# Optimization experiments

Hardware: AMD Instinct MI355X
Metric: run time of the kernel (lower is better)

The kernel has to match this reference:

```python
import jax, jax.numpy as jnp
import numpy as np

NUM_ENTITIES = 40000
NUM_RELATIONS = 500
NUM_EDGES = 400000
ENT_DIM = 50
REL_DIM = 50
NUM_HEADS = 8
UNITS = [150, 300]
NEG_SLOPE = 0.2


def setup_inputs() -> dict:
    key = jax.random.key(0)
    ks = jax.random.split(key, 12)
    h_index = jax.random.randint(ks[0], (NUM_EDGES,), 0, NUM_ENTITIES)
    r_index = jax.random.randint(ks[1], (NUM_EDGES,), 0, NUM_RELATIONS)
    t_index = jax.random.randint(ks[2], (NUM_EDGES,), 0, NUM_ENTITIES)
    std_e = np.sqrt(1.0 / ENT_DIM).astype(np.float32)
    std_r = np.sqrt(1.0 / REL_DIM).astype(np.float32)
    entity_embeddings = jax.random.truncated_normal(ks[3], -2.0, 2.0, (NUM_ENTITIES, ENT_DIM), jnp.float32) * std_e
    relation_embeddings = jax.random.truncated_normal(ks[4], -2.0, 2.0, (NUM_RELATIONS, REL_DIM), jnp.float32) * std_r
    # gat0: input ent dim 50, rel dim 50 -> concat 150, units 150
    c0 = ENT_DIM + REL_DIM + ENT_DIM
    gat0_kernel = jax.random.normal(ks[5], (NUM_HEADS, c0, UNITS[0]), jnp.float32) * (1.0 / np.sqrt(c0))
    gat0_attn = jax.random.normal(ks[6], (NUM_HEADS, UNITS[0]), jnp.float32) * (1.0 / np.sqrt(UNITS[0]))
    gat0_rel_kernel = jax.random.normal(ks[7], (REL_DIM, UNITS[0]), jnp.float32) * (1.0 / np.sqrt(REL_DIM))
    # gat1: input ent dim 8*150=1200, rel dim 150 -> concat 2550, units 300
    e1 = NUM_HEADS * UNITS[0]
    c1 = e1 + UNITS[0] + e1
    gat1_kernel = jax.random.normal(ks[8], (NUM_HEADS, c1, UNITS[1]), jnp.float32) * (1.0 / np.sqrt(c1))
    gat1_attn = jax.random.normal(ks[9], (NUM_HEADS, UNITS[1]), jnp.float32) * (1.0 / np.sqrt(UNITS[1]))
    gat1_rel_kernel = jax.random.normal(ks[10], (UNITS[0], UNITS[1]), jnp.float32) * (1.0 / np.sqrt(UNITS[0]))
    dense_w = jax.random.normal(ks[11], (ENT_DIM, UNITS[1]), jnp.float32) * (1.0 / np.sqrt(ENT_DIM))
    dense_b = jnp.zeros((UNITS[1],), jnp.float32)
    return dict(h_index=h_index, r_index=r_index, t_index=t_index,
                entity_embeddings=entity_embeddings, relation_embeddings=relation_embeddings,
                gat0_kernel=gat0_kernel, gat0_attn=gat0_attn, gat0_rel_kernel=gat0_rel_kernel,
                gat1_kernel=gat1_kernel, gat1_attn=gat1_attn, gat1_rel_kernel=gat1_rel_kernel,
                dense_w=dense_w, dense_b=dense_b)


def _kbgat_layer(h, r, t, ent, rel, kernel, attn, rel_kernel):
    """One KBGAT layer. kernel: [H, De+Dr+De, U] acting on concat(ent[h], rel[r], ent[t]).
    Split kernel so projections happen at node/relation level (equivalent, avoids E x concat_dim)."""
    N = ent.shape[0]
    De = ent.shape[1]
    Dr = rel.shape[1]
    outs = []
    for hd in range(kernel.shape[0]):
        W = kernel[hd]
        Wh, Wr, Wt = W[:De], W[De:De + Dr], W[De + Dr:]
        # message c_{hrt} = W [ent_h ; rel_r ; ent_t] : [E, U]
        c = (ent @ Wh)[h] + (rel @ Wr)[r] + (ent @ Wt)[t]
        s = jax.nn.leaky_relu(c @ attn[hd], NEG_SLOPE)  # [E]
        # segment softmax over triples sharing the same head entity
        m = jax.ops.segment_max(s, h, num_segments=N)
        e = jnp.exp(s - m[h])
        d = jax.ops.segment_sum(e, h, num_segments=N)
        a = e / (d[h] + 1e-10)
        agg = jax.ops.segment_sum(a[:, None] * c, h, num_segments=N)  # [N, U]
        outs.append(jax.nn.elu(agg))
    rel_out = rel @ rel_kernel
    return outs, rel_out


def reference(h_index, r_index, t_index, entity_embeddings, relation_embeddings,
              gat0_kernel, gat0_attn, gat0_rel_kernel,
              gat1_kernel, gat1_attn, gat1_rel_kernel, dense_w, dense_b):
    h = h_index.astype(jnp.int32)
    r = r_index.astype(jnp.int32)
    t = t_index.astype(jnp.int32)
    # dropout rate is 0.0 / inference -> identity
    outs0, rel0 = _kbgat_layer(h, r, t, entity_embeddings, relation_embeddings,
                               gat0_kernel, gat0_attn, gat0_rel_kernel)
    feat = jnp.concatenate(outs0, axis=-1)  # [N, H*U0]
    outs1, rel1 = _kbgat_layer(h, r, t, feat, rel0, gat1_kernel, gat1_attn, gat1_rel_kernel)
    ent_out = outs1[0]
    for o in outs1[1:]:
        ent_out = ent_out + o  # add_n over heads
    ent_out = ent_out + (entity_embeddings @ dense_w + dense_b)  # dense residual
    return ent_out, rel1
```

## Files before the change

### kernel.cpp

```cpp
#include <hip/hip_runtime.h>
#include <hip/hip_bf16.h>
#include <math.h>
#include <stdint.h>

typedef __attribute__((ext_vector_type(8))) __bf16 bf16x8;
typedef __attribute__((ext_vector_type(4))) float f32x4;
typedef unsigned short us;

#define GLP(p) ((__attribute__((address_space(1))) void*)(p))
#define LDP(p) ((__attribute__((address_space(3))) void*)(p))

static __device__ __forceinline__ float b2f(us u) {
    return __uint_as_float(((unsigned int)u) << 16);
}
static __device__ __forceinline__ us f2b(float f) {
    unsigned int x = __float_as_uint(f);
    return (us)((x + 0x7fffu + ((x >> 16) & 1u)) >> 16);
}

__global__ __launch_bounds__(256) void sentinel(float* out, int n, float v) {
    int i = blockIdx.x * 256 + threadIdx.x;
    if (i < n) out[i] = v;
}

__global__ __launch_bounds__(256) void zero_featpad(us* __restrict__ feat) {
    int idx = blockIdx.x * 256 + threadIdx.x;
    if (idx < 40064 * 16) {
        int n = idx >> 4, c = idx & 15;
        feat[(size_t)n * 1216 + 1200 + c] = 0;
    }
}
__global__ __launch_bounds__(256) void zero_x0pad(us* __restrict__ X0) {
    int idx = blockIdx.x * 256 + threadIdx.x;
    if (idx < 4 * 64 * 192) {
        int w = idx / (64 * 192);
        int rem = idx % (64 * 192);
        int rr = rem / 192, c = rem % 192;
        X0[((size_t)w * 40064 + 40000 + rr) * 192 + c] = 0;
    }
}

__global__ __launch_bounds__(256) void count_edges(const int* __restrict__ h, int* __restrict__ counts) {
    int e = blockIdx.x * 256 + threadIdx.x;
    if (e < 400000) atomicAdd(&counts[h[e]], 1);
}

__global__ void scan40k(const int* __restrict__ counts, int* __restrict__ rs) {
    __shared__ int part[1024];
    int tid = threadIdx.x;
    int base = tid * 40;
    int s = 0;
    for (int i = 0; i < 40; ++i) { int idx = base + i; s += (idx < 40000) ? counts[idx] : 0; }
    part[tid] = s;
    __syncthreads();
    for (int off = 1; off < 1024; off <<= 1) {
        int v = (tid >= off) ? part[tid - off] : 0;
        __syncthreads();
        part[tid] += v;
        __syncthreads();
    }
    int run = (tid == 0) ? 0 : part[tid - 1];
    for (int i = 0; i < 40; ++i) {
        int idx = base + i;
        if (idx < 40000) { rs[idx] = run; run += counts[idx]; }
    }
    if (tid == 1023) rs[40000] = part[1023];
}

__global__ __launch_bounds__(256) void scatter_edges(const int* __restrict__ h, const int* __restrict__ rs,
                                                     int* __restrict__ cursor, int* __restrict__ se) {
    int e = blockIdx.x * 256 + threadIdx.x;
    if (e < 400000) {
        int n = h[e];
        int pos = rs[n] + atomicAdd(&cursor[n], 1);
        se[pos] = e;
    }
}

__global__ __launch_bounds__(256) void pack_ent(const float* __restrict__ ent, us* __restrict__ A0) {
    int idx = blockIdx.x * 256 + threadIdx.x;
    if (idx >= 40064 * 64) return;
    int n = idx >> 6, k = idx & 63;
    A0[idx] = (n < 40000 && k < 50) ? f2b(ent[n * 50 + k]) : (us)0;
}

__global__ __launch_bounds__(256) void build_V0(const float* __restrict__ g0k, const float* __restrict__ attn0,
                                                float* __restrict__ V0) {
    int idx = blockIdx.x * 256 + threadIdx.x;
    if (idx >= 50 * 24) return;
    int k = idx / 24, g = idx % 24;
    int part = g >> 3, hd = g & 7;
    int row = k + (part == 1 ? 100 : (part == 2 ? 50 : 0));
    float s = 0.f;
    for (int u = 0; u < 150; ++u)
        s += g0k[(hd * 150 + row) * 150 + u] * attn0[hd * 150 + u];
    V0[idx] = s;
}

__global__ __launch_bounds__(256) void build_VT0(const float* __restrict__ g0k, const float* __restrict__ attn0,
                                                 us* __restrict__ VT0) {
    int idx = blockIdx.x * 256 + threadIdx.x;
    if (idx >= 128 * 64) return;
    int g = idx >> 6, k = idx & 63;
    us v = 0;
    if (g < 16 && k < 50) {
        int part = g >> 3, hd = g & 7;
        int row = part ? (100 + k) : k;
        float s = 0.f;
        for (int u = 0; u < 150; ++u)
            s += g0k[(hd * 150 + row) * 150 + u] * attn0[hd * 150 + u];
        v = f2b(s);
    }
    VT0[idx] = v;
}

__global__ __launch_bounds__(256) void build_VT1(const float* __restrict__ g1k, const float* __restrict__ attn1,
                                                 us* __restrict__ VT1) {
    int idx = blockIdx.x * 256 + threadIdx.x;
    if (idx >= 128 * 1216) return;
    int g = idx / 1216, k = idx % 1216;
    us v = 0;
    if (g < 16 && k < 1200) {
        int part = g >> 3, hd = g & 7;
        int row = part ? (1350 + k) : k;
        float s = 0.f;
        for (int u = 0; u < 300; ++u)
            s += g1k[((size_t)hd * 2550 + row) * 300 + u] * attn1[hd * 300 + u];
        v = f2b(s);
    }
    VT1[idx] = v;
}

__global__ __launch_bounds__(256) void build_Vr1(const float* __restrict__ g1k, const float* __restrict__ attn1,
                                                 float* __restrict__ Vr1) {
    int idx = blockIdx.x * 256 + threadIdx.x;
    if (idx >= 150 * 8) return;
    int k = idx / 8, hd = idx % 8;
    float s = 0.f;
    for (int u = 0; u < 300; ++u)
        s += g1k[((size_t)hd * 2550 + 1200 + k) * 300 + u] * attn1[hd * 300 + u];
    Vr1[idx] = s;
}

__global__ __launch_bounds__(256) void build_dwT(const float* __restrict__ dw, us* __restrict__ dwT) {
    int idx = blockIdx.x * 256 + threadIdx.x;
    if (idx >= 384 * 64) return;
    int j = idx >> 6, k = idx & 63;
    us v = 0;
    if (j < 300 && k < 50) v = f2b(dw[k * 300 + j]);
    dwT[idx] = v;
}

__global__ __launch_bounds__(256) void scalar_proj(const void* __restrict__ Av, int aIsF32, int lda, int K,
                                                   const float* __restrict__ V, int ldv, int col0, int G,
                                                   float* __restrict__ out) {
    __shared__ float arow[1216];
    long n = blockIdx.x;
    if (aIsF32) {
        const float* A = (const float*)Av;
        for (int k = threadIdx.x; k < K; k += 256) arow[k] = A[n * lda + k];
    } else {
        const us* A = (const us*)Av;
        for (int k = threadIdx.x; k < K; k += 256) arow[k] = b2f(A[n * lda + k]);
    }
    __syncthreads();
    int g = threadIdx.x >> 4;
    int sl = threadIdx.x & 15;
    if (g < G) {
        float s = 0.f;
        for (int k = sl; k < K; k += 16) s += arow[k] * V[k * ldv + col0 + g];
        for (int off = 8; off; off >>= 1) s += __shfl_down(s, off, 16);
        if (sl == 0) out[n * G + g] = s;
    }
}

__global__ __launch_bounds__(256) void edge_stats2(const int* __restrict__ rs, const int* __restrict__ se,
                                                   const int* __restrict__ rIdx, const int* __restrict__ tIdx,
                                                   const float* __restrict__ sc, const float* __restrict__ arr,
                                                   us* __restrict__ eAT, float* __restrict__ sfac,
                                                   float* __restrict__ sS) {
    int tid = blockIdx.x * 256 + threadIdx.x;
    if (tid >= 40000 * 8) return;
    int n = tid >> 3, hd = tid & 7;
    float ah = sc[n * 16 + hd];
    int p0 = rs[n], p1 = rs[n + 1];
    float m = -INFINITY, d = 0.f;
    for (int p = p0; p < p1; ++p) {
        int e = se[p];
        float s = ah + arr[rIdx[e] * 8 + hd] + sc[tIdx[e] * 16 + 8 + hd];
        s = (s > 0.f) ? s : 0.2f * s;
        sS[(size_t)p * 8 + hd] = s;
        if (s > m) { d = d * expf(m - s) + 1.f; m = s; }
        else d += expf(s - m);
    }
    float inv = 1.f / (d + 1e-10f);
    us* ea = eAT + (size_t)hd * 400000;
    for (int p = p0; p < p1; ++p) {
        float s = sS[(size_t)p * 8 + hd];
        ea[p] = f2b(expf(s - m) * inv);
    }
    sfac[tid] = d * inv;
}

__global__ __launch_bounds__(256) void agg0x4(int g, const int* __restrict__ rs, const int* __restrict__ se,
                                              const int* __restrict__ rIdx, const int* __restrict__ tIdx,
                                              const us* __restrict__ eAT, const float* __restrict__ sfac,
                                              const float* __restrict__ ent, const float* __restrict__ rel,
                                              us* __restrict__ X0) {
    __shared__ int sr[128], st[128];
    __shared__ float sa[4][128];
    long n = blockIdx.x;
    int tid = threadIdx.x;
    int lane = tid & 63, wave = tid >> 6;
    int hd = 4 * g + wave;
    int k = lane;
    float ev = (k < 50) ? ent[n * 50 + k] : 0.f;
    float xh = sfac[n * 8 + hd] * ev;
    float ra = 0.f, ta = 0.f;
    int p0 = rs[n], p1 = rs[n + 1];
    for (int c0 = p0; c0 < p1; c0 += 128) {
        int cnt = min(128, p1 - c0);
        __syncthreads();
        if (tid < cnt) {
            int e = se[c0 + tid];
            sr[tid] = rIdx[e];
            st[tid] = tIdx[e];
#pragma unroll
            for (int w = 0; w < 4; ++w)
                sa[w][tid] = b2f(eAT[(size_t)(4 * g + w) * 400000 + c0 + tid]);
        }
        __syncthreads();
#pragma unroll 4
        for (int i = 0; i < cnt; ++i) {
            float a = sa[wave][i];
            int r = sr[i], t = st[i];
            if (k < 50) {
                ra += a * rel[r * 50 + k];
                ta += a * ent[(long)t * 50 + k];
            }
        }
    }
    us* row = X0 + ((size_t)wave * 40064 + n) * 192;
    if (k < 50) { row[k] = f2b(xh); row[50 + k] = f2b(ra); row[100 + k] = f2b(ta); }
    if (lane < 42) row[150 + lane] = 0;
}

__global__ __launch_bounds__(256) void build_B0T8(const float* __restrict__ g0k, us* __restrict__ B) {
    int idx = blockIdx.x * 256 + threadIdx.x;
    if (idx >= 8 * 256 * 192) return;
    int hd = idx / (256 * 192);
    int u = (idx / 192) % 256, k = idx % 192;
    us v = 0;
    if (u < 150 && k < 150) v = f2b(g0k[((size_t)hd * 150 + k) * 150 + u]);
    B[idx] = v;
}

__global__ __launch_bounds__(256) void build_B1Th2T(int g, const float* __restrict__ g1k, us* __restrict__ B) {
    __shared__ us tile[64][65];
    int j0 = blockIdx.x * 64, k0 = blockIdx.y * 64;
    int tl = threadIdx.x & 63, th = threadIdx.x >> 6;
#pragma unroll 4
    for (int i = 0; i < 16; ++i) {
        int jj = j0 + tl;
        int kk = k0 + th + 4 * i;
        us v = 0;
        if (jj < 1216 && kk < 1200) {
            int blk = jj / 304, u = jj % 304;
            if (u < 300) {
                int hd = 2 * g + (blk & 1);
                int row = (blk >= 2) ? (1350 + kk) : kk;
                v = f2b(g1k[((size_t)hd * 2550 + row) * 300 + u]);
            }
        }
        tile[tl][th + 4 * i] = v;
    }
    __syncthreads();
#pragma unroll 4
    for (int i = 0; i < 16; ++i) {
        int k = k0 + tl;
        int j = j0 + th + 4 * i;
        if (j < 1280 && k < 1216) B[(size_t)j * 1216 + k] = tile[th + 4 * i][tl];
    }
}

#define GEMM_BODY(EPILOG)                                                                       \
    __shared__ __align__(16) us As[2][128 * 64];                                                \
    __shared__ __align__(16) us Bs[2][128 * 64];                                                \
    const int tid = threadIdx.x;                                                                \
    const int lane = tid & 63, wave = tid >> 6;                                                 \
    const int wr = wave >> 1, wc = wave & 1;                                                    \
    const int r16 = lane & 15, g4 = lane >> 4;                                                  \
    const int gx = gridDim.x;                                                                   \
    const int nwg = gx * gridDim.y;                                                             \
    const int orig = blockIdx.y * gx + blockIdx.x;                                              \
    const int q8 = nwg >> 3, r8 = nwg & 7;                                                      \
    const int xcd = orig & 7;                                                                   \
    const int lg = (xcd < r8 ? xcd * (q8 + 1) : r8 * (q8 + 1) + (xcd - r8) * q8) + (orig >> 3); \
    const long bm = lg / gx, bn = lg % gx;                                                      \
    f32x4 acc[4][4];                                                                            \
    _Pragma("unroll") for (int m = 0; m < 4; ++m)                                               \
        _Pragma("unroll") for (int n = 0; n < 4; ++n) acc[m][n] = (f32x4){0.f, 0.f, 0.f, 0.f};  \
    auto stage = [&](int buf, int kt) {                                                         \
        _Pragma("unroll") for (int i = 0; i < 4; ++i) {                                         \
            int idx = tid + i * 256;                                                            \
            int row = idx >> 3, sub = idx & 7;                                                  \
            int scol = ((sub ^ (row & 7)) << 3);                                                \
            const us* ga = A + (bm * 128 + row) * (long)K + kt + scol;                          \
            __builtin_amdgcn_global_load_lds(GLP(ga), LDP(&As[buf][idx * 8]), 16, 0, 0);        \
        }                                                                                       \
        _Pragma("unroll") for (int i = 0; i < 4; ++i) {                                         \
            int idx = tid + i * 256;                                                            \
            int row = idx >> 3, sub = idx & 7;                                                  \
            int scol = ((sub ^ (row & 7)) << 3);                                                \
            const us* gb = BT + (bn * 128 + row) * (long)K + kt + scol;                         \
            __builtin_amdgcn_global_load_lds(GLP(gb), LDP(&Bs[buf][idx * 8]), 16, 0, 0);        \
        }                                                                                       \
    };                                                                                          \
    const int nt = K >> 6;                                                                      \
    stage(0, 0);                                                                                \
    const int sxor = (r16 & 7) << 3;                                                            \
    for (int t = 0; t < nt; ++t) {                                                              \
        int cur = t & 1;                                                                        \
        if (t + 1 < nt) {                                                                       \
            stage(cur ^ 1, (t + 1) << 6);                                                       \
            asm volatile("s_waitcnt vmcnt(8)" ::: "memory");                                    \
        } else {                                                                                \
            asm volatile("s_waitcnt vmcnt(0)" ::: "memory");                                    \
        }                                                                                       \
        __builtin_amdgcn_s_barrier();                                                           \
        asm volatile("" ::: "memory");                                                          \
        __builtin_amdgcn_s_setprio(1);                                                          \
        _Pragma("unroll") for (int kk = 0; kk < 2; ++kk) {                                      \
            bf16x8 af[4], bfr[4];                                                               \
            _Pragma("unroll") for (int m = 0; m < 4; ++m)                                       \
                af[m] = *(const bf16x8*)&As[cur][(wr * 64 + m * 16 + r16) * 64 +                \
                                               ((kk * 32 + g4 * 8) ^ sxor)];                    \
            _Pragma("unroll") for (int n = 0; n < 4; ++n)                                       \
                bfr[n] = *(const bf16x8*)&Bs[cur][(wc * 64 + n * 16 + r16) * 64 +               \
                                                ((kk * 32 + g4 * 8) ^ sxor)];                   \
            _Pragma("unroll") for (int m = 0; m < 4; ++m)                                       \
                _Pragma("unroll") for (int n = 0; n < 4; ++n)                                   \
                    acc[m][n] = __builtin_amdgcn_mfma_f32_16x16x32_bf16(af[m], bfr[n],          \
                                                                        acc[m][n], 0, 0, 0);    \
        }                                                                                       \
        __builtin_amdgcn_s_setprio(0);                                                          \
        asm volatile("" ::: "memory");                                                          \
        __builtin_amdgcn_s_barrier();                                                           \
    }                                                                                           \
    _Pragma("unroll") for (int m = 0; m < 4; ++m)                                               \
        _Pragma("unroll") for (int n = 0; n < 4; ++n)                                           \
            _Pragma("unroll") for (int j = 0; j < 4; ++j) { EPILOG }

__global__ __launch_bounds__(256) void gemm_bt(const us* __restrict__ A_, const us* __restrict__ BT_,
                                               us* __restrict__ C, int K, int ldc, int nColReal,
                                               int colOff0, int colOffZ, long aStrideZ, long btStrideZ,
                                               int act) {
    const int z = blockIdx.z;
    const us* A = A_ + (size_t)z * aStrideZ;
    const us* BT = BT_ + (size_t)z * btStrideZ;
    const int colBase = colOff0 + z * colOffZ;
    GEMM_BODY(
        int cc = (int)bn * 128 + wc * 64 + n * 16 + r16;
        if (cc < nColReal) {
            long row = bm * 128 + wr * 64 + m * 16 + g4 * 4 + j;
            float v = acc[m][n][j];
            if (act) v = (v > 0.f) ? v : expm1f(v);
            C[row * (long)ldc + colBase + cc] = f2b(v);
        })
}

__global__ __launch_bounds__(256) void gemm_bt_f32(const us* __restrict__ A, const us* __restrict__ BT,
                                                   float* __restrict__ C, int K, int ldc, int nColReal,
                                                   const float* __restrict__ bias) {
    GEMM_BODY(
        int cc = (int)bn * 128 + wc * 64 + n * 16 + r16;
        if (cc < nColReal) {
            long row = bm * 128 + wr * 64 + m * 16 + g4 * 4 + j;
            float v = acc[m][n][j];
            if (bias) v += bias[cc];
            C[row * (long)ldc + cc] = v;
        })
}

__global__ __launch_bounds__(256) void rel0_kernel(const float* __restrict__ rel, const float* __restrict__ g0rk,
                                                   float* __restrict__ rel0b) {
    int idx = blockIdx.x * 256 + threadIdx.x;
    if (idx >= 500 * 150) return;
    int rI = idx / 150, u = idx % 150;
    float s = 0.f;
    for (int k = 0; k < 50; ++k) s += rel[rI * 50 + k] * g0rk[k * 150 + u];
    rel0b[idx] = s;
}

__global__ __launch_bounds__(256) void pr1_kernel(const float* __restrict__ rel0b, const float* __restrict__ g1k,
                                                  us* __restrict__ PR1b) {
    int idx = blockIdx.x * 256 + threadIdx.x;
    if (idx >= 500 * 2400) return;
    int rI = idx / 2400, jj = idx % 2400;
    int hd = jj / 300, u = jj % 300;
    float s = 0.f;
    for (int k = 0; k < 150; ++k)
        s += rel0b[rI * 150 + k] * g1k[((size_t)hd * 2550 + 1200 + k) * 300 + u];
    PR1b[idx] = f2b(s);
}

__global__ __launch_bounds__(256) void rel1_kernel(const float* __restrict__ rel0b, const float* __restrict__ g1rk,
                                                   float* __restrict__ out) {
    int idx = blockIdx.x * 256 + threadIdx.x;
    if (idx >= 500 * 300) return;
    int rI = idx / 300, u = idx % 300;
    float s = 0.f;
    for (int k = 0; k < 150; ++k) s += rel0b[rI * 150 + k] * g1rk[k * 300 + u];
    out[idx] = s;
}

__global__ __launch_bounds__(256) void agg1h2(int g, const int* __restrict__ rs, const int* __restrict__ se,
                                              const int* __restrict__ rIdx, const int* __restrict__ tIdx,
                                              const us* __restrict__ eAT, const float* __restrict__ sfac,
                                              const us* __restrict__ C1g2, const us* __restrict__ PR1b,
                                              float* __restrict__ outf) {
    __shared__ int sr[128], st[128];
    __shared__ float sa0[128], sa1[128];
    long n = blockIdx.x;
    int tid = threadIdx.x;
    int hd0 = 2 * g, hd1 = hd0 + 1;
    int d = tid, d2 = tid + 256;
    bool a2 = (d2 < 300);
    float sf0 = sfac[n * 8 + hd0], sf1 = sfac[n * 8 + hd1];
    const us* crow = C1g2 + (size_t)n * 1216;
    float acc00 = sf0 * b2f(crow[d]);
    float acc10 = sf1 * b2f(crow[304 + d]);
    float acc01 = a2 ? sf0 * b2f(crow[d2]) : 0.f;
    float acc11 = a2 ? sf1 * b2f(crow[304 + d2]) : 0.f;
    const us* ea0 = eAT + (size_t)hd0 * 400000;
    const us* ea1 = eAT + (size_t)hd1 * 400000;
    int p0 = rs[n], p1 = rs[n + 1];
    for (int c0 = p0; c0 < p1; c0 += 128) {
        int cnt = min(128, p1 - c0);
        __syncthreads();
        if (tid < cnt) {
            int e = se[c0 + tid];
            sr[tid] = rIdx[e];
            st[tid] = tIdx[e];
            sa0[tid] = b2f(ea0[c0 + tid]);
            sa1[tid] = b2f(ea1[c0 + tid]);
        }
        __syncthreads();
#pragma unroll 4
        for (int i = 0; i < cnt; ++i) {
            int r = sr[i], t = st[i];
            float a0 = sa0[i], a1 = sa1[i];
            const us* ct = C1g2 + (size_t)t * 1216;
            const us* pr = PR1b + (size_t)r * 2400;
            acc00 += a0 * (b2f(pr[hd0 * 300 + d]) + b2f(ct[608 + d]));
            acc10 += a1 * (b2f(pr[hd1 * 300 + d]) + b2f(ct[912 + d]));
            if (a2) {
                acc01 += a0 * (b2f(pr[hd0 * 300 + d2]) + b2f(ct[608 + d2]));
                acc11 += a1 * (b2f(pr[hd1 * 300 + d2]) + b2f(ct[912 + d2]));
            }
        }
    }
    float v00 = (acc00 > 0.f) ? acc00 : expm1f(acc00);
    float v10 = (acc10 > 0.f) ? acc10 : expm1f(acc10);
    outf[n * 300 + d] += v00 + v10;
    if (a2) {
        float v01 = (acc01 > 0.f) ? acc01 : expm1f(acc01);
        float v11 = (acc11 > 0.f) ? acc11 : expm1f(acc11);
        outf[n * 300 + d2] += v01 + v11;
    }
}

extern "C" void kernel_launch(void* const* d_in, const int* in_sizes, int n_in,
                              void* d_out, int out_size, void* d_ws, size_t ws_size,
                              hipStream_t stream) {
    const int* hIdx = (const int*)d_in[0];
    const int* rIdx = (const int*)d_in[1];
    const int* tIdx = (const int*)d_in[2];
    const float* ent  = (const float*)d_in[3];
    const float* rel  = (const float*)d_in[4];
    const float* g0k  = (const float*)d_in[5];
    const float* at0w = (const float*)d_in[6];
    const float* g0rk = (const float*)d_in[7];
    const float* g1k  = (const float*)d_in[8];
    const float* at1w = (const float*)d_in[9];
    const float* g1rk = (const float*)d_in[10];
    const float* dw   = (const float*)d_in[11];
    const float* db   = (const float*)d_in[12];
    float* outf = (float*)d_out;

    {
        const int exp_sz[13] = {400000, 400000, 400000, 2000000, 25000, 180000, 1200,
                                7500, 6120000, 2400, 45000, 15000, 300};
        bool ok = (n_in == 13);
        for (int i = 0; ok && i < 13; ++i) ok = (in_sizes[i] == exp_sz[i]);
        if (!ok) {
            sentinel<<<(out_size + 255) / 256, 256, 0, stream>>>(outf, out_size, 44.0f);
            return;
        }
    }

    char* p = (char*)d_ws;
    auto carve = [&](size_t bytes) -> char* {
        char* r = p;
        p += (bytes + 255) & ~(size_t)255;
        return r;
    };
    int* counts = (int*)carve(40000 * 4);
    int* cursor = (int*)carve(40000 * 4);
    int* rs     = (int*)carve(40001 * 4);
    int* se     = (int*)carve(400000 * 4);
    float* sc   = (float*)carve((size_t)40064 * 16 * 4);
    float* arS  = (float*)carve(500 * 8 * 4);
    us* eAT     = (us*)carve((size_t)8 * 400000 * 2);
    float* sfac = (float*)carve((size_t)40000 * 8 * 4);
    float* V0  = (float*)carve(50 * 24 * 4);
    float* Vr1 = (float*)carve(150 * 8 * 4);
    float* rel0b = (float*)carve(500 * 150 * 4);
    us* PR1b  = (us*)carve((size_t)500 * 2400 * 2);
    us* VT0   = (us*)carve((size_t)128 * 64 * 2);
    us* VT1   = (us*)carve((size_t)128 * 1216 * 2);
    us* dwT   = (us*)carve((size_t)384 * 64 * 2);
    us* B0T8  = (us*)carve((size_t)8 * 256 * 192 * 2);
    us* B1Th2 = (us*)carve((size_t)1280 * 1216 * 2);
    us* feat  = (us*)carve((size_t)40064 * 1216 * 2);
    char* tail = p;
    us* A0    = (us*)tail;
    float* sS = (float*)tail;
    us* X0    = (us*)tail;
    us* C1g2  = (us*)tail;
    size_t tailNeed = (size_t)40064 * 1216 * 2;
    size_t totalNeed = (size_t)(tail - (char*)d_ws) + tailNeed;
    if (totalNeed > ws_size) {
        sentinel<<<(out_size + 255) / 256, 256, 0, stream>>>(outf, out_size, 42.0f);
        return;
    }

    hipMemsetAsync(counts, 0, 40000 * 4, stream);
    hipMemsetAsync(cursor, 0, 40000 * 4, stream);
    zero_featpad<<<(40064 * 16 + 255) / 256, 256, 0, stream>>>(feat);

    count_edges<<<1563, 256, 0, stream>>>(hIdx, counts);
    scan40k<<<1, 1024, 0, stream>>>(counts, rs);
    scatter_edges<<<1563, 256, 0, stream>>>(hIdx, rs, cursor, se);

    pack_ent<<<(40064 * 64 + 255) / 256, 256, 0, stream>>>(ent, A0);
    build_VT0<<<(128 * 64 + 255) / 256, 256, 0, stream>>>(g0k, at0w, VT0);
    gemm_bt_f32<<<dim3(1, 313), 256, 0, stream>>>(A0, VT0, sc, 64, 16, 16, nullptr);
    build_dwT<<<(384 * 64 + 255) / 256, 256, 0, stream>>>(dw, dwT);
    gemm_bt_f32<<<dim3(3, 313), 256, 0, stream>>>(A0, dwT, outf, 64, 300, 300, db);
    build_V0<<<5, 256, 0, stream>>>(g0k, at0w, V0);
    scalar_proj<<<500, 256, 0, stream>>>(rel, 1, 50, 50, V0, 24, 16, 8, arS);
    edge_stats2<<<1250, 256, 0, stream>>>(rs, se, rIdx, tIdx, sc, arS, eAT, sfac, sS);

    zero_x0pad<<<(4 * 64 * 192 + 255) / 256, 256, 0, stream>>>(X0);
    build_B0T8<<<(8 * 256 * 192 + 255) / 256, 256, 0, stream>>>(g0k, B0T8);
    for (int g = 0; g < 2; ++g) {
        agg0x4<<<40000, 256, 0, stream>>>(g, rs, se, rIdx, tIdx, eAT, sfac, ent, rel, X0);
        gemm_bt<<<dim3(2, 313, 4), 256, 0, stream>>>(X0, B0T8 + (size_t)g * 4 * 256 * 192, feat,
                                                     192, 1216, 150, g * 600, 150,
                                                     (long)40064 * 192, (long)256 * 192, 1);
    }

    rel0_kernel<<<(500 * 150 + 255) / 256, 256, 0, stream>>>(rel, g0rk, rel0b);
    build_VT1<<<(128 * 1216 + 255) / 256, 256, 0, stream>>>(g1k, at1w, VT1);
    build_Vr1<<<5, 256, 0, stream>>>(g1k, at1w, Vr1);
    gemm_bt_f32<<<dim3(1, 313), 256, 0, stream>>>(feat, VT1, sc, 1216, 16, 16, nullptr);
    scalar_proj<<<500, 256, 0, stream>>>(rel0b, 1, 150, 150, Vr1, 8, 0, 8, arS);
    edge_stats2<<<1250, 256, 0, stream>>>(rs, se, rIdx, tIdx, sc, arS, eAT, sfac, sS);
    pr1_kernel<<<(500 * 2400 + 255) / 256, 256, 0, stream>>>(rel0b, g1k, PR1b);

    for (int g = 0; g < 4; ++g) {
        build_B1Th2T<<<dim3(20, 19), 256, 0, stream>>>(g, g1k, B1Th2);
        gemm_bt<<<dim3(10, 313, 1), 256, 0, stream>>>(feat, B1Th2, C1g2,
                                                      1216, 1216, 1216, 0, 0, 0, 0, 0);
        agg1h2<<<40000, 256, 0, stream>>>(g, rs, se, rIdx, tIdx, eAT, sfac, C1g2, PR1b, outf);
    }

    rel1_kernel<<<(500 * 300 + 255) / 256, 256, 0, stream>>>(rel0b, g1rk, outf + (size_t)40000 * 300);
}
```

Baseline: 1.941 ms.

## Map one wavefront per node in both aggregation kernels, dropping LDS staging

Both edge-aggregation kernels now give each wavefront its own destination node, four nodes per block, instead of one node per 256-thread block. The layer-0 kernel has each wave accumulate all four heads for its node, so each relation and tail row is loaded once and reused across heads. The layer-1 kernel has each lane own five contiguous output columns. The shared-memory edge staging and __syncthreads barriers are removed, along with idle threads on low-degree nodes. In exchange, the layer-1 loads of five contiguous bf16 values per lane are strided across lanes and less coalesced, and edge metadata is re-read by every lane.

After: 2.506 ms. +29.1%, slower.

```diff
diff --git a/kernel.cpp b/kernel.cpp
--- a/kernel.cpp
+++ b/kernel.cpp
@@ -202,47 +202,40 @@
     sfac[tid] = d * inv;
 }
 
-__global__ __launch_bounds__(256) void agg0x4(int g, const int* __restrict__ rs, const int* __restrict__ se,
-                                              const int* __restrict__ rIdx, const int* __restrict__ tIdx,
-                                              const us* __restrict__ eAT, const float* __restrict__ sfac,
-                                              const float* __restrict__ ent, const float* __restrict__ rel,
-                                              us* __restrict__ X0) {
-    __shared__ int sr[128], st[128];
-    __shared__ float sa[4][128];
-    long n = blockIdx.x;
-    int tid = threadIdx.x;
-    int lane = tid & 63, wave = tid >> 6;
-    int hd = 4 * g + wave;
+__global__ __launch_bounds__(256) void agg0x4w(int g, const int* __restrict__ rs, const int* __restrict__ se,
+                                               const int* __restrict__ rIdx, const int* __restrict__ tIdx,
+                                               const us* __restrict__ eAT, const float* __restrict__ sfac,
+                                               const float* __restrict__ ent, const float* __restrict__ rel,
+                                               us* __restrict__ X0) {
+    int wave = threadIdx.x >> 6, lane = threadIdx.x & 63;
+    long n = (long)blockIdx.x * 4 + wave;
     int k = lane;
     float ev = (k < 50) ? ent[n * 50 + k] : 0.f;
-    float xh = sfac[n * 8 + hd] * ev;
-    float ra = 0.f, ta = 0.f;
+    float ra[4] = {0.f, 0.f, 0.f, 0.f}, ta[4] = {0.f, 0.f, 0.f, 0.f};
+    const us* ea0 = eAT + (size_t)(4 * g + 0) * 400000;
+    const us* ea1 = eAT + (size_t)(4 * g + 1) * 400000;
+    const us* ea2 = eAT + (size_t)(4 * g + 2) * 400000;
+    const us* ea3 = eAT + (size_t)(4 * g + 3) * 400000;
     int p0 = rs[n], p1 = rs[n + 1];
-    for (int c0 = p0; c0 < p1; c0 += 128) {
-        int cnt = min(128, p1 - c0);
-        __syncthreads();
-        if (tid < cnt) {
-            int e = se[c0 + tid];
-            sr[tid] = rIdx[e];
-            st[tid] = tIdx[e];
+#pragma unroll 2
+    for (int p = p0; p < p1; ++p) {
+        int e = se[p];
+        long r = rIdx[e], t = tIdx[e];
+        float a0 = b2f(ea0[p]), a1 = b2f(ea1[p]), a2 = b2f(ea2[p]), a3 = b2f(ea3[p]);
+        if (k < 50) {
+            float rv = rel[r * 50 + k];
+            float tv = ent[t * 50 + k];
+            ra[0] += a0 * rv; ra[1] += a1 * rv; ra[2] += a2 * rv; ra[3] += a3 * rv;
+            ta[0] += a0 * tv; ta[1] += a1 * tv; ta[2] += a2 * tv; ta[3] += a3 * tv;
+        }
+    }
 #pragma unroll
-            for (int w = 0; w < 4; ++w)
-                sa[w][tid] = b2f(eAT[(size_t)(4 * g + w) * 400000 + c0 + tid]);
-        }
-        __syncthreads();
-#pragma unroll 4
-        for (int i = 0; i < cnt; ++i) {
-            float a = sa[wave][i];
-            int r = sr[i], t = st[i];
-            if (k < 50) {
-                ra += a * rel[r * 50 + k];
-                ta += a * ent[(long)t * 50 + k];
-            }
-        }
-    }
-    us* row = X0 + ((size_t)wave * 40064 + n) * 192;
-    if (k < 50) { row[k] = f2b(xh); row[50 + k] = f2b(ra); row[100 + k] = f2b(ta); }
-    if (lane < 42) row[150 + lane] = 0;
+    for (int w = 0; w < 4; ++w) {
+        us* row = X0 + ((size_t)w * 40064 + n) * 192;
+        float xh = sfac[n * 8 + 4 * g + w] * ev;
+        if (k < 50) { row[k] = f2b(xh); row[50 + k] = f2b(ra[w]); row[100 + k] = f2b(ta[w]); }
+        if (lane < 42) row[150 + lane] = 0;
+    }
 }
 
 __global__ __launch_bounds__(256) void build_B0T8(const float* __restrict__ g0k, us* __restrict__ B) {
@@ -414,60 +407,54 @@
     out[idx] = s;
 }
 
-__global__ __launch_bounds__(256) void agg1h2(int g, const int* __restrict__ rs, const int* __restrict__ se,
-                                              const int* __restrict__ rIdx, const int* __restrict__ tIdx,
-                                              const us* __restrict__ eAT, const float* __restrict__ sfac,
-                                              const us* __restrict__ C1g2, const us* __restrict__ PR1b,
-                                              float* __restrict__ outf) {
-    __shared__ int sr[128], st[128];
-    __shared__ float sa0[128], sa1[128];
-    long n = blockIdx.x;
-    int tid = threadIdx.x;
+__global__ __launch_bounds__(256) void agg1h2w(int g, const int* __restrict__ rs, const int* __restrict__ se,
+                                               const int* __restrict__ rIdx, const int* __restrict__ tIdx,
+                                               const us* __restrict__ eAT, const float* __restrict__ sfac,
+                                               const us* __restrict__ C1g2, const us* __restrict__ PR1b,
+                                               float* __restrict__ outf) {
+    int wave = threadIdx.x >> 6, lane = threadIdx.x & 63;
+    long n = (long)blockIdx.x * 4 + wave;
     int hd0 = 2 * g, hd1 = hd0 + 1;
-    int d = tid, d2 = tid + 256;
-    bool a2 = (d2 < 300);
+    int d0 = lane * 5;
+    int nd = 300 - d0;
+    nd = (nd < 0) ? 0 : ((nd > 5) ? 5 : nd);
     float sf0 = sfac[n * 8 + hd0], sf1 = sfac[n * 8 + hd1];
     const us* crow = C1g2 + (size_t)n * 1216;
-    float acc00 = sf0 * b2f(crow[d]);
-    float acc10 = sf1 * b2f(crow[304 + d]);
-    float acc01 = a2 ? sf0 * b2f(crow[d2]) : 0.f;
-    float acc11 = a2 ? sf1 * b2f(crow[304 + d2]) : 0.f;
+    float acc0[5], acc1[5];
+#pragma unroll
+    for (int q = 0; q < 5; ++q) { acc0[q] = 0.f; acc1[q] = 0.f; }
+#pragma unroll
+    for (int q = 0; q < 5; ++q)
+        if (q < nd) {
+            acc0[q] = sf0 * b2f(crow[d0 + q]);
+            acc1[q] = sf1 * b2f(crow[304 + d0 + q]);
+        }
     const us* ea0 = eAT + (size_t)hd0 * 400000;
     const us* ea1 = eAT + (size_t)hd1 * 400000;
     int p0 = rs[n], p1 = rs[n + 1];
-    for (int c0 = p0; c0 < p1; c0 += 128) {
-        int cnt = min(128, p1 - c0);
-        __syncthreads();
-        if (tid < cnt) {
-            int e = se[c0 + tid];
-            sr[tid] = rIdx[e];
-            st[tid] = tIdx[e];
-            sa0[tid] = b2f(ea0[c0 + tid]);
-            sa1[tid] = b2f(ea1[c0 + tid]);
+#pragma unroll 2
+    for (int p = p0; p < p1; ++p) {
+        int e = se[p];
+        long r = rIdx[e], t = tIdx[e];
+        float a0 = b2f(ea0[p]), a1 = b2f(ea1[p]);
+        const us* ct = C1g2 + (size_t)t * 1216;
+        const us* pr = PR1b + (size_t)r * 2400;
+#pragma unroll
+        for (int q = 0; q < 5; ++q)
+            if (q < nd) {
+                int d = d0 + q;
+                acc0[q] += a0 * (b2f(pr[hd0 * 300 + d]) + b2f(ct[608 + d]));
+                acc1[q] += a1 * (b2f(pr[hd1 * 300 + d]) + b2f(ct[912 + d]));
+            }
+    }
+#pragma unroll
+    for (int q = 0; q < 5; ++q)
+        if (q < nd) {
+            float v0 = acc0[q], v1 = acc1[q];
+            v0 = (v0 > 0.f) ? v0 : expm1f(v0);
+            v1 = (v1 > 0.f) ? v1 : expm1f(v1);
+            outf[n * 300 + d0 + q] += v0 + v1;
         }
-        __syncthreads();
-#pragma unroll 4
-        for (int i = 0; i < cnt; ++i) {
-            int r = sr[i], t = st[i];
-            float a0 = sa0[i], a1 = sa1[i];
-            const us* ct = C1g2 + (size_t)t * 1216;
-            const us* pr = PR1b + (size_t)r * 2400;
-            acc00 += a0 * (b2f(pr[hd0 * 300 + d]) + b2f(ct[608 + d]));
-            acc10 += a1 * (b2f(pr[hd1 * 300 + d]) + b2f(ct[912 + d]));
-            if (a2) {
-                acc01 += a0 * (b2f(pr[hd0 * 300 + d2]) + b2f(ct[608 + d2]));
-                acc11 += a1 * (b2f(pr[hd1 * 300 + d2]) + b2f(ct[912 + d2]));
-            }
-        }
-    }
-    float v00 = (acc00 > 0.f) ? acc00 : expm1f(acc00);
-    float v10 = (acc10 > 0.f) ? acc10 : expm1f(acc10);
-    outf[n * 300 + d] += v00 + v10;
-    if (a2) {
-        float v01 = (acc01 > 0.f) ? acc01 : expm1f(acc01);
-        float v11 = (acc11 > 0.f) ? acc11 : expm1f(acc11);
-        outf[n * 300 + d2] += v01 + v11;
-    }
 }
 
 extern "C" void kernel_launch(void* const* d_in, const int* in_sizes, int n_in,
@@ -555,7 +542,7 @@
     zero_x0pad<<<(4 * 64 * 192 + 255) / 256, 256, 0, stream>>>(X0);
     build_B0T8<<<(8 * 256 * 192 + 255) / 256, 256, 0, stream>>>(g0k, B0T8);
     for (int g = 0; g < 2; ++g) {
-        agg0x4<<<40000, 256, 0, stream>>>(g, rs, se, rIdx, tIdx, eAT, sfac, ent, rel, X0);
+        agg0x4w<<<10000, 256, 0, stream>>>(g, rs, se, rIdx, tIdx, eAT, sfac, ent, rel, X0);
         gemm_bt<<<dim3(2, 313, 4), 256, 0, stream>>>(X0, B0T8 + (size_t)g * 4 * 256 * 192, feat,
                                                      192, 1216, 150, g * 600, 150,
                                                      (long)40064 * 192, (long)256 * 192, 1);
@@ -573,7 +560,7 @@
         build_B1Th2T<<<dim3(20, 19), 256, 0, stream>>>(g, g1k, B1Th2);
         gemm_bt<<<dim3(10, 313, 1), 256, 0, stream>>>(feat, B1Th2, C1g2,
                                                       1216, 1216, 1216, 0, 0, 0, 0, 0);
-        agg1h2<<<40000, 256, 0, stream>>>(g, rs, se, rIdx, tIdx, eAT, sfac, C1g2, PR1b, outf);
+        agg1h2w<<<10000, 256, 0, stream>>>(g, rs, se, rIdx, tIdx, eAT, sfac, C1g2, PR1b, outf);
     }
 
     rel1_kernel<<<(500 * 300 + 255) / 256, 256, 0, stream>>>(rel0b, g1rk, outf + (size_t)40000 * 300);
```
